# Optimization experiments

Measured on AMD Instinct MI355X. Metric: run time of the kernel, lower is better.

Reference implementation:

```python
import jax, jax.numpy as jnp
import numpy as np

N, E, G, H, ED, L = 100000, 256000, 4000, 300, 64, 5
BN_EPS = 1e-5


def _bn(x, p):
    # p: [4, D] = (gamma, beta, running_mean, running_var); eval-mode batchnorm
    g, b, m, v = p[0], p[1], p[2], p[3]
    return (x - m) * (g / jnp.sqrt(v + BN_EPS)) + b


def setup_inputs() -> dict:
    key = jax.random.key(0)
    ks = iter(jax.random.split(key, 64))
    r = lambda *s: jax.random.normal(next(ks), s, jnp.float32) * 0.02

    def bn_pack(*s):
        # stacked (gamma, beta, mean, var) along axis -2
        return jnp.stack([jnp.ones(s, jnp.float32), jnp.zeros(s, jnp.float32),
                          jax.random.normal(next(ks), s, jnp.float32) * 0.1,
                          jnp.ones(s, jnp.float32)], axis=-2)

    inp = {
        'x': jax.random.randint(next(ks), (N,), 0, 119),
        'edge_attr': jax.random.randint(next(ks), (E,), 0, 32),
        'edge_index': jax.random.randint(next(ks), (2, E), 0, N),
        'batch': jnp.sort(jax.random.randint(next(ks), (N,), 0, G)),
        'num_graphs': G,
        # encoders
        'atom_emb': r(119, H), 'bond_emb': r(32, ED),
        # per-layer GINEConv params (stacked over L layers)
        'We': r(L, H, ED), 'be': jnp.zeros((L, H)),              # edge Linear(edge_dim->hidden)
        'W1': r(L, 2 * H, H), 'b1': jnp.zeros((L, 2 * H)), 'bn1': bn_pack(L, 2 * H),
        'W2': r(L, H, 2 * H), 'b2': jnp.zeros((L, H)), 'bn2': bn_pack(L, H),
        'eps': jnp.zeros((L,), jnp.float32),                      # trainable GIN eps, init 0
        # per-layer pooling linear
        'Wp': r(L, H, H), 'bp': jnp.zeros((L, H)),
        # virtual-node update MLP
        'vnW1': r(H, H), 'vnb1': jnp.zeros((H,)), 'vnbn': bn_pack(H),
        'vnW2': r(H, H), 'vnb2': jnp.zeros((H,)),
        # readout layernorm + head (Linear(H,H//2) -> SiLU -> Linear(H//2,1))
        'ln_g': jnp.ones((H,)), 'ln_b': jnp.zeros((H,)),
        'hW1': r(H // 2, H), 'hb1': jnp.zeros((H // 2,)),
        'hW2': r(1, H // 2), 'hb2': jnp.zeros((1,)),
    }
    return inp


def reference(x, edge_attr, edge_index, batch, num_graphs, atom_emb, bond_emb,
              We, be, W1, b1, bn1, W2, b2, bn2, eps, Wp, bp,
              vnW1, vnb1, vnbn, vnW2, vnb2, ln_g, ln_b, hW1, hb1, hW2, hb2):
    Gn = num_graphs
    h = atom_emb[x]                         # [N, H] atom encoding
    e = bond_emb[edge_attr]                 # [E, ED] bond encoding
    src, dst = edge_index[0], edge_index[1]
    Nn, Hd = h.shape
    vn = jnp.zeros((Gn, Hd), h.dtype)       # vn_embedding init to 0
    hg = jnp.zeros((Gn, Hd), h.dtype)       # sum-over-layers graph readout
    nlayers = We.shape[0]
    for i in range(nlayers):
        if i > 0:
            # virtual-node update + broadcast
            vn_in = jax.ops.segment_sum(h, batch, num_segments=Gn) + vn
            vn = jax.nn.silu(_bn(vn_in @ vnW1.T + vnb1, vnbn)) @ vnW2.T + vnb2
            h = h + vn[batch]
        # GINEConv: sum_j ReLU(h_j + lin(e_ij)) scattered into target nodes
        ep = e @ We[i].T + be[i]             # [E, H]
        m = jax.nn.relu(h[src] + ep)         # gather + relu
        agg = jax.ops.segment_sum(m, dst, num_segments=Nn)  # scatter-add
        z = (1.0 + eps[i]) * h + agg
        z = jax.nn.silu(_bn(z @ W1[i].T + b1[i], bn1[i])) @ W2[i].T + b2[i]  # 2-layer MLP
        z = jax.nn.silu(_bn(z, bn2[i]))      # layer BN + SiLU
        h = z + h if i > 0 else z            # residual (skipped at layer 0)
        hp = jax.ops.segment_sum(h, batch, num_segments=Gn)  # global_add_pool
        hg = hg + hp @ Wp[i].T + bp[i]
    # readout: LayerNorm -> SiLU -> head MLP
    mu = hg.mean(-1, keepdims=True)
    var = ((hg - mu) ** 2).mean(-1, keepdims=True)
    r = jax.nn.silu((hg - mu) / jnp.sqrt(var + BN_EPS) * ln_g + ln_b)
    return jax.nn.silu(r @ hW1.T + hb1) @ hW2.T + hb2   # [G, 1]
```

## Files before the change

### kernel.cpp

```cpp
#include <hip/hip_runtime.h>
#include <hip/hip_bf16.h>
#include <math.h>


typedef __hip_bfloat16 bf16;
typedef __attribute__((ext_vector_type(8))) __bf16 bf16x8;
typedef __attribute__((ext_vector_type(4))) float f32x4;

__device__ __forceinline__ float silu_f(float v) { return v / (1.0f + __expf(-v)); }
__device__ __forceinline__ float bfu_lo(unsigned u) {
    unsigned t = (u & 0xffffu) << 16; return *(float*)&t;
}
__device__ __forceinline__ float bfu_hi(unsigned u) {
    unsigned t = u & 0xffff0000u; return *(float*)&t;
}
__device__ __forceinline__ unsigned packbf(float a, float b) {
    bf16 x = __float2bfloat16(a), y = __float2bfloat16(b);
    return (unsigned)*(unsigned short*)&x | ((unsigned)*(unsigned short*)&y << 16);
}

#define GLOAD16(gp, lp) __builtin_amdgcn_global_load_lds( \
    (const __attribute__((address_space(1))) unsigned int*)(const void*)(gp), \
    (__attribute__((address_space(3))) unsigned int*)(void*)(lp), 16, 0, 0)

__global__ void k_fill(float* __restrict__ p, float v, int n) {
    int stride = gridDim.x * blockDim.x;
    for (int i = blockIdx.x * blockDim.x + threadIdx.x; i < n; i += stride) p[i] = v;
}

__global__ void k_zero(float* __restrict__ p, size_t n) {
    size_t stride = (size_t)gridDim.x * blockDim.x;
    for (size_t i = (size_t)blockIdx.x * blockDim.x + threadIdx.x; i < n; i += stride)
        p[i] = 0.0f;
}

__global__ void k_hist(const int* __restrict__ key, int* __restrict__ cnt, int n) {
    int stride = gridDim.x * blockDim.x;
    for (int i = blockIdx.x * blockDim.x + threadIdx.x; i < n; i += stride)
        atomicAdd(&cnt[key[i]], 1);
}

__global__ __launch_bounds__(256)
void k_scan1(const int* __restrict__ in, int* __restrict__ out,
             int* __restrict__ bsum, int n) {
    __shared__ int wsum[4];
    int base = blockIdx.x << 10;
    int t = threadIdx.x;
    int i0 = base + t * 4;
    int v0 = (i0 + 0 < n) ? in[i0 + 0] : 0;
    int v1 = (i0 + 1 < n) ? in[i0 + 1] : 0;
    int v2 = (i0 + 2 < n) ? in[i0 + 2] : 0;
    int v3 = (i0 + 3 < n) ? in[i0 + 3] : 0;
    int s = v0 + v1 + v2 + v3;
    int lane = t & 63, wid = t >> 6;
    int x = s;
    for (int d = 1; d < 64; d <<= 1) {
        int y = __shfl_up(x, d);
        if (lane >= d) x += y;
    }
    if (lane == 63) wsum[wid] = x;
    __syncthreads();
    int wadd = 0;
    for (int w = 0; w < wid; w++) wadd += wsum[w];
    x += wadd;
    int run = x - s;
    if (i0 + 0 < n) out[i0 + 0] = run; run += v0;
    if (i0 + 1 < n) out[i0 + 1] = run; run += v1;
    if (i0 + 2 < n) out[i0 + 2] = run; run += v2;
    if (i0 + 3 < n) out[i0 + 3] = run; run += v3;
    if (bsum && t == 255) bsum[blockIdx.x] = x;
}

__global__ void k_scan_add(int* __restrict__ out, const int* __restrict__ bsum,
                           int* __restrict__ cur, int n, int total) {
    int stride = gridDim.x * blockDim.x;
    for (int i = blockIdx.x * blockDim.x + threadIdx.x; i < n; i += stride) {
        int v = out[i] + bsum[i >> 10];
        out[i] = v;
        if (cur) cur[i] = v;
    }
    if (blockIdx.x == 0 && threadIdx.x == 0) out[n] = total;
}

__global__ void k_escatter(const int* __restrict__ dst, const int* __restrict__ src,
                           const int* __restrict__ ea, int* __restrict__ cur,
                           int* __restrict__ esrc, int* __restrict__ eea, int E) {
    int stride = gridDim.x * blockDim.x;
    for (int e = blockIdx.x * blockDim.x + threadIdx.x; e < E; e += stride) {
        int p = atomicAdd(&cur[dst[e]], 1);
        esrc[p] = src[e];
        eea[p]  = ea[e];
    }
}

__global__ void k_eptable(const float* __restrict__ bond_emb,
                          const float* __restrict__ We,
                          const float* __restrict__ be,
                          bf16* __restrict__ tblb, int BV, int H, int ED, int KP1) {
    int l = blockIdx.x / BV;
    int a = blockIdx.x % BV;
    int j = threadIdx.x;
    if (j >= KP1) return;
    float s = 0.0f;
    if (j < H) {
        const float* w = We + ((size_t)l * H + j) * ED;
        const float* bb = bond_emb + (size_t)a * ED;
        s = be[(size_t)l * H + j];
        for (int k = 0; k < ED; k++) s += bb[k] * w[k];
    }
    tblb[((size_t)l * BV + a) * KP1 + j] = __float2bfloat16(s);
}

__global__ void k_encode(const int* __restrict__ x, const float* __restrict__ emb,
                         bf16* __restrict__ h, int H, int total) {
    int stride = gridDim.x * blockDim.x;
    for (int i = blockIdx.x * blockDim.x + threadIdx.x; i < total; i += stride) {
        int n = i / H, j = i - n * H;
        h[i] = __float2bfloat16(emb[(size_t)x[n] * H + j]);
    }
}

__global__ __launch_bounds__(256)
void k_msg_csr(const int* __restrict__ eoff, const int* __restrict__ esrc,
               const int* __restrict__ eea, const bf16* __restrict__ h,
               const bf16* __restrict__ tblb, const float* __restrict__ epsp, int l,
               bf16* __restrict__ zb, int H, int KP1, int N) {
    const int wid = blockIdx.x * (blockDim.x >> 6) + (threadIdx.x >> 6);
    const int nw = gridDim.x * (blockDim.x >> 6);
    const int lane = threadIdx.x & 63;
    const float epl = 1.0f + epsp[l];
    const int c0 = 2 * lane;
    for (int n = wid; n < N; n += nw) {
        int e0 = eoff[n], e1 = eoff[n + 1];
        float a0[3] = {0.f, 0.f, 0.f}, a1[3] = {0.f, 0.f, 0.f};
        for (int e = e0; e < e1; e++) {
            int s = esrc[e], a = eea[e];
            const unsigned short* hr = (const unsigned short*)h + (size_t)s * H;
            const unsigned short* tr = (const unsigned short*)tblb + (size_t)a * KP1;
            #pragma unroll
            for (int p = 0; p < 3; p++) {
                int c = c0 + p * 128;
                if (c < H) {
                    unsigned hv = *(const unsigned*)(hr + c);
                    unsigned tv = *(const unsigned*)(tr + c);
                    float v0 = bfu_lo(hv) + bfu_lo(tv);
                    float v1 = bfu_hi(hv) + bfu_hi(tv);
                    if (v0 > 0.0f) a0[p] += v0;
                    if (v1 > 0.0f) a1[p] += v1;
                }
            }
        }
        const unsigned short* hn = (const unsigned short*)h + (size_t)n * H;
        unsigned short* zr = (unsigned short*)zb + (size_t)n * KP1;
        #pragma unroll
        for (int p = 0; p < 3; p++) {
            int c = c0 + p * 128;
            if (c < KP1) {
                float z0 = 0.f, z1 = 0.f;
                if (c < H) {
                    unsigned hv = *(const unsigned*)(hn + c);
                    z0 = epl * bfu_lo(hv) + a0[p];
                    z1 = epl * bfu_hi(hv) + a1[p];
                }
                *(unsigned*)(zr + c) = packbf(z0, z1);
            }
        }
    }
}

__global__ __launch_bounds__(256)
void k_pool_csr(const int* __restrict__ goff, const bf16* __restrict__ h,
                float* __restrict__ hp, bf16* __restrict__ hps, int layer, int KPS,
                int H, int G) {
    int j = threadIdx.x;
    int c = 2 * j;
    if (c >= H) return;
    for (int g = blockIdx.x; g < G; g += gridDim.x) {
        float s0 = 0.0f, s1 = 0.0f;
        int n0 = goff[g], n1 = goff[g + 1];
        const unsigned short* hb = (const unsigned short*)h;
        for (int n = n0; n < n1; n++) {
            unsigned hv = *(const unsigned*)(hb + (size_t)n * H + c);
            s0 += bfu_lo(hv);
            s1 += bfu_hi(hv);
        }
        hp[(size_t)g * H + c] = s0;
        hp[(size_t)g * H + c + 1] = s1;
        *(unsigned*)((unsigned short*)hps + (size_t)g * KPS + layer * H + c) = packbf(s0, s1);
    }
}

__global__ void k_addvn(bf16* __restrict__ h, const float* __restrict__ vn,
                        const int* __restrict__ batch, int H, int total2) {
    int stride = gridDim.x * blockDim.x;
    int HP = H >> 1;
    for (int i = blockIdx.x * blockDim.x + threadIdx.x; i < total2; i += stride) {
        int n = i / HP, p = i - n * HP;
        int c = 2 * p;
        unsigned short* hr = (unsigned short*)h + (size_t)n * H + c;
        unsigned hv = *(unsigned*)hr;
        const float* vr = vn + (size_t)batch[n] * H + c;
        *(unsigned*)hr = packbf(bfu_lo(hv) + vr[0], bfu_hi(hv) + vr[1]);
    }
}

__global__ void k_add_castpad(const float* __restrict__ hp, const float* __restrict__ vn,
                              bf16* __restrict__ o, int H, int KP, int total) {
    int stride = gridDim.x * blockDim.x;
    for (int i = blockIdx.x * blockDim.x + threadIdx.x; i < total; i += stride) {
        int g = i / KP, c = i - g * KP;
        float v = 0.0f;
        if (c < H) v = hp[(size_t)g * H + c] + vn[(size_t)g * H + c];
        o[i] = __float2bfloat16(v);
    }
}

__global__ void k_castw_all(const float* __restrict__ W, bf16* __restrict__ Wb,
                            int L, int R, int K, int Kp, int total) {
    int stride = gridDim.x * blockDim.x;
    int perL = R * K;
    for (int i = blockIdx.x * blockDim.x + threadIdx.x; i < total; i += stride) {
        int RpKp = total / L;
        int l = i / RpKp, rem = i - l * RpKp;
        int r = rem / Kp, c = rem - r * Kp;
        float v = (r < R && c < K) ? W[(size_t)l * perL + (size_t)r * K + c] : 0.0f;
        Wb[i] = __float2bfloat16(v);
    }
}

__global__ void k_castWps(const float* __restrict__ Wp, bf16* __restrict__ Wb,
                          int L, int H, int KPS, int total) {
    int stride = gridDim.x * blockDim.x;
    for (int i = blockIdx.x * blockDim.x + threadIdx.x; i < total; i += stride) {
        int r = i / KPS, c = i - r * KPS;
        float v = 0.0f;
        if (r < H && c < L * H) {
            int li = c / H, k = c - li * H;
            v = Wp[(size_t)li * H * H + (size_t)r * H + k];
        }
        Wb[i] = __float2bfloat16(v);
    }
}

__global__ void k_sumbias(const float* __restrict__ bp, float* __restrict__ o,
                          int L, int H) {
    int j = blockIdx.x * blockDim.x + threadIdx.x;
    if (j < H) {
        float s = 0.f;
        for (int i = 0; i < L; i++) s += bp[(size_t)i * H + j];
        o[j] = s;
    }
}

__global__ __launch_bounds__(512)
void k_mfma_gemm(const bf16* __restrict__ A, const bf16* __restrict__ B,
                 const float* __restrict__ bias, const float* __restrict__ bn,
                 const bf16* __restrict__ resb, bf16* __restrict__ out,
                 float* __restrict__ outf,
                 int M, int Nc, int Kp, int ldA, int ldOut, int ldPad,
                 int dosilu, int ncol) {
    __shared__ short As[3 * 128 * 32];
    __shared__ short Bs[3 * 128 * 32];
    const int nwg = gridDim.x;
    const int bid = blockIdx.x;
    const int q = nwg >> 3, r = nwg & 7;
    const int xcd = bid & 7, ii = bid >> 3;
    const int wgid = (xcd < r ? xcd * (q + 1) : r * (q + 1) + (xcd - r) * q) + ii;
    const int rb = wgid / ncol, cb = wgid - rb * ncol;
    const int bm = rb * 128, bn0 = cb * 128;

    const int tid = threadIdx.x;
    const int wave = tid >> 6, lane = tid & 63;
    const int wr = wave >> 1, wc = wave & 1;
    const int l15 = lane & 15, l4 = lane >> 4;
    const int srow = wave * 16 + (lane >> 2);
    const int sslot = lane & 3;

    f32x4 acc[2][4];
    #pragma unroll
    for (int mi = 0; mi < 2; mi++)
        #pragma unroll
        for (int ni = 0; ni < 4; ni++)
            acc[mi][ni] = (f32x4){0.f, 0.f, 0.f, 0.f};

    const int sg = (sslot ^ ((srow >> 1) & 3)) << 3;

    auto STAGE = [&](int buf, int k0) {
        GLOAD16(A + (size_t)(bm + srow) * ldA + k0 + sg, As + buf * 4096 + wave * 512);
        GLOAD16(B + (size_t)(bn0 + srow) * Kp + k0 + sg, Bs + buf * 4096 + wave * 512);
    };

    const int nt = Kp >> 5;
    STAGE(0, 0);
    if (nt > 1) STAGE(1, 32);
    for (int t = 0; t < nt; ++t) {
        if (t + 1 < nt) asm volatile("s_waitcnt vmcnt(2)" ::: "memory");
        else            asm volatile("s_waitcnt vmcnt(0)" ::: "memory");
        __builtin_amdgcn_sched_barrier(0);
        __builtin_amdgcn_s_barrier();
        __builtin_amdgcn_sched_barrier(0);
        if (t + 2 < nt) STAGE((t + 2) % 3, (t + 2) << 5);
        const short* Ab = As + (t % 3) * 4096;
        const short* Bb = Bs + (t % 3) * 4096;
        bf16x8 a[2], b[4];
        #pragma unroll
        for (int mi = 0; mi < 2; mi++) {
            int row = wr * 32 + mi * 16 + l15;
            a[mi] = *(const bf16x8*)&Ab[row * 32 + ((l4 ^ ((row >> 1) & 3)) << 3)];
        }
        #pragma unroll
        for (int ni = 0; ni < 4; ni++) {
            int row = wc * 64 + ni * 16 + l15;
            b[ni] = *(const bf16x8*)&Bb[row * 32 + ((l4 ^ ((row >> 1) & 3)) << 3)];
        }
        #pragma unroll
        for (int mi = 0; mi < 2; mi++)
            #pragma unroll
            for (int ni = 0; ni < 4; ni++)
                acc[mi][ni] = __builtin_amdgcn_mfma_f32_16x16x32_bf16(
                    a[mi], b[ni], acc[mi][ni], 0, 0, 0);
        __builtin_amdgcn_sched_barrier(0);
    }

    #pragma unroll
    for (int ni = 0; ni < 4; ni++) {
        int col = bn0 + wc * 64 + ni * 16 + l15;
        if (col >= ldPad) continue;
        bool pad = (col >= Nc);
        float bi = (!pad && bias) ? bias[col] : 0.f;
        float sc = 1.f, mm = 0.f, bb = 0.f;
        if (!pad && bn) {
            sc = bn[col] * rsqrtf(bn[3 * Nc + col] + 1e-5f);
            mm = bn[2 * Nc + col];
            bb = bn[Nc + col];
        }
        #pragma unroll
        for (int mi = 0; mi < 2; mi++) {
            #pragma unroll
            for (int rr = 0; rr < 4; rr++) {
                int row = bm + wr * 32 + mi * 16 + l4 * 4 + rr;
                if (row >= M) continue;
                size_t idx = (size_t)row * ldOut + col;
                if (outf) {
                    if (pad) continue;
                    float v = acc[mi][ni][rr] + bi;
                    if (bn) v = (v - mm) * sc + bb;
                    if (dosilu) v = silu_f(v);
                    outf[idx] = v;
                } else {
                    if (pad) { out[idx] = __float2bfloat16(0.f); continue; }
                    float v = acc[mi][ni][rr] + bi;
                    if (bn) v = (v - mm) * sc + bb;
                    if (dosilu) v = silu_f(v);
                    if (resb) v += __bfloat162float(resb[idx]);
                    out[idx] = __float2bfloat16(v);
                }
            }
        }
    }
}

#define GBM 64
#define GBN 64
#define GBK 16
__global__ __launch_bounds__(256)
void k_gemm(const float* __restrict__ A, const float* __restrict__ B,
            const float* __restrict__ bias, const float* __restrict__ bn,
            float* __restrict__ C, int M, int Nc, int K, int flags) {
    __shared__ float As[GBK][GBM + 4];
    __shared__ float Bs[GBK][GBN + 4];
    const int bm = blockIdx.x * GBM;
    const int bnc = blockIdx.y * GBN;
    const int tid = threadIdx.x;
    const int tx = tid & 15, ty = tid >> 4;
    const int ar = tid >> 2;
    const int ak = (tid & 3) << 2;

    float acc[4][4] = {{0.f}};

    for (int k0 = 0; k0 < K; k0 += GBK) {
        {
            int gr = bm + ar, gk = k0 + ak;
            float4 v = make_float4(0.f, 0.f, 0.f, 0.f);
            if (gr < M && gk < K) {
                const float* p = A + (size_t)gr * K;
                if (gk + 3 < K) v = *(const float4*)(p + gk);
                else {
                    v.x = p[gk];
                    if (gk + 1 < K) v.y = p[gk + 1];
                    if (gk + 2 < K) v.z = p[gk + 2];
                }
            }
            As[ak][ar] = v.x; As[ak + 1][ar] = v.y; As[ak + 2][ar] = v.z; As[ak + 3][ar] = v.w;
        }
        {
            int gr = bnc + ar, gk = k0 + ak;
            float4 v = make_float4(0.f, 0.f, 0.f, 0.f);
            if (gr < Nc && gk < K) {
                const float* p = B + (size_t)gr * K;
                if (gk + 3 < K) v = *(const float4*)(p + gk);
                else {
                    v.x = p[gk];
                    if (gk + 1 < K) v.y = p[gk + 1];
                    if (gk + 2 < K) v.z = p[gk + 2];
                }
            }
            Bs[ak][ar] = v.x; Bs[ak + 1][ar] = v.y; Bs[ak + 2][ar] = v.z; Bs[ak + 3][ar] = v.w;
        }
        __syncthreads();
        #pragma unroll
        for (int kk = 0; kk < GBK; kk++) {
            float4 a = *(const float4*)&As[kk][ty * 4];
            float4 b = *(const float4*)&Bs[kk][tx * 4];
            acc[0][0] += a.x * b.x; acc[0][1] += a.x * b.y; acc[0][2] += a.x * b.z; acc[0][3] += a.x * b.w;
            acc[1][0] += a.y * b.x; acc[1][1] += a.y * b.y; acc[1][2] += a.y * b.z; acc[1][3] += a.y * b.w;
            acc[2][0] += a.z * b.x; acc[2][1] += a.z * b.y; acc[2][2] += a.z * b.z; acc[2][3] += a.z * b.w;
            acc[3][0] += a.w * b.x; acc[3][1] += a.w * b.y; acc[3][2] += a.w * b.z; acc[3][3] += a.w * b.w;
        }
        __syncthreads();
    }

    #pragma unroll
    for (int i = 0; i < 4; i++) {
        int row = bm + ty * 4 + i;
        if (row >= M) continue;
        #pragma unroll
        for (int j = 0; j < 4; j++) {
            int col = bnc + tx * 4 + j;
            if (col >= Nc) continue;
            float v = acc[i][j];
            if (bias) v += bias[col];
            if (bn) {
                float g = bn[col], bb = bn[Nc + col], mm = bn[2 * Nc + col], vv = bn[3 * Nc + col];
                v = (v - mm) * (g * rsqrtf(vv + 1e-5f)) + bb;
            }
            if (flags & 1) v = silu_f(v);
            size_t idx = (size_t)row * Nc + col;
            if (flags & 2) C[idx] += v;
            else           C[idx] = v;
        }
    }
}

__global__ __launch_bounds__(256)
void k_ln_silu(const float* __restrict__ hg, const float* __restrict__ g,
               const float* __restrict__ b, float* __restrict__ r, int H) {
    int gi = blockIdx.x;
    const float* row = hg + (size_t)gi * H;
    float s = 0.f, s2 = 0.f;
    for (int j = threadIdx.x; j < H; j += blockDim.x) {
        float v = row[j];
        s += v; s2 += v * v;
    }
    for (int off = 32; off; off >>= 1) {
        s += __shfl_down(s, off);
        s2 += __shfl_down(s2, off);
    }
    __shared__ float rs[4], rs2[4];
    int wid = threadIdx.x >> 6, lane = threadIdx.x & 63;
    if (lane == 0) { rs[wid] = s; rs2[wid] = s2; }
    __syncthreads();
    if (threadIdx.x == 0) {
        float S = 0.f, S2 = 0.f;
        for (int w = 0; w < 4; w++) { S += rs[w]; S2 += rs2[w]; }
        rs[0] = S; rs2[0] = S2;
    }
    __syncthreads();
    float mu = rs[0] / H;
    float var = rs2[0] / H - mu * mu;
    float inv = rsqrtf(var + 1e-5f);
    for (int j = threadIdx.x; j < H; j += blockDim.x) {
        float v = (row[j] - mu) * inv * g[j] + b[j];
        r[(size_t)gi * H + j] = silu_f(v);
    }
}

__global__ void k_head2(const float* __restrict__ r2, const float* __restrict__ w,
                        const float* __restrict__ b, float* __restrict__ out, int Kh) {
    int gi = blockIdx.x;
    int t = threadIdx.x;
    float s = 0.f;
    for (int k = t; k < Kh; k += 64) s += r2[(size_t)gi * Kh + k] * w[k];
    for (int off = 32; off; off >>= 1) s += __shfl_down(s, off);
    if (t == 0) out[gi] = s + b[0];
}

extern "C" void kernel_launch(void* const* d_in, const int* in_sizes, int n_in,
                              void* d_out, int out_size, void* d_ws, size_t ws_size,
                              hipStream_t stream) {
    const int*   x         = (const int*)d_in[0];
    const int*   edge_attr = (const int*)d_in[1];
    const int*   eidx      = (const int*)d_in[2];
    const int*   batch     = (const int*)d_in[3];
    const float* atom_emb  = (const float*)d_in[5];
    const float* bond_emb  = (const float*)d_in[6];
    const float* We  = (const float*)d_in[7];
    const float* be  = (const float*)d_in[8];
    const float* W1  = (const float*)d_in[9];
    const float* b1  = (const float*)d_in[10];
    const float* bn1 = (const float*)d_in[11];
    const float* W2  = (const float*)d_in[12];
    const float* b2  = (const float*)d_in[13];
    const float* bn2 = (const float*)d_in[14];
    const float* epsp= (const float*)d_in[15];
    const float* Wp  = (const float*)d_in[16];
    const float* bp  = (const float*)d_in[17];
    const float* vnW1= (const float*)d_in[18];
    const float* vnb1= (const float*)d_in[19];
    const float* vnbn= (const float*)d_in[20];
    const float* vnW2= (const float*)d_in[21];
    const float* vnb2= (const float*)d_in[22];
    const float* ln_g= (const float*)d_in[23];
    const float* ln_b= (const float*)d_in[24];
    const float* hW1 = (const float*)d_in[25];
    const float* hb1 = (const float*)d_in[26];
    const float* hW2 = (const float*)d_in[27];
    const float* hb2 = (const float*)d_in[28];
    float* out = (float*)d_out;

    const int N  = in_sizes[0];
    const int E  = in_sizes[1];
    const int G  = out_size;
    const int L  = in_sizes[15];
    const int H  = in_sizes[19];
    const int H2 = 2 * H;
    const int ED = in_sizes[7] / (L * H);
    const int BV = in_sizes[6] / ED;
    const int HH = in_sizes[26];
    (void)n_in;

    const int* src = eidx;
    const int* dst = eidx + E;

    const int KP1 = ((H  + 31) / 32) * 32;
    const int KP2 = ((H2 + 31) / 32) * 32;
    const int KPS = ((L * H + 31) / 32) * 32;
    const int RP1 = ((H2 + 127) / 128) * 128;
    const int RP2 = ((H  + 127) / 128) * 128;
    const int Npad = ((N + 127) / 128) * 128;
    const int GP   = ((G + 127) / 128) * 128;

    char* wsb = (char*)d_ws;
    auto alb = [](size_t v) { return (v + 255) & ~(size_t)255; };
    const size_t fN = (size_t)N * H;
    const size_t fG = (size_t)G * H;

    size_t off = 0;
    bf16*  hbf   = (bf16*) (wsb + off); off += alb(fN * 2);
    bf16*  zb    = (bf16*) (wsb + off); off += alb((size_t)Npad * KP1 * 2);
    float* hp    = (float*)(wsb + off); off += alb(fG * 4);
    float* hg    = (float*)(wsb + off); off += alb(fG * 4);
    float* vn    = (float*)(wsb + off); off += alb(fG * 4);
    float* rbuf  = (float*)(wsb + off); off += alb(fG * 4);
    float* r2    = (float*)(wsb + off); off += alb((size_t)G * HH * 4);
    bf16*  tblb  = (bf16*) (wsb + off); off += alb((size_t)L * BV * KP1 * 2);
    float* bsumf = (float*)(wsb + off); off += alb((size_t)RP2 * 4);
    bf16*  W1b   = (bf16*) (wsb + off); off += alb((size_t)L * RP1 * KP1 * 2);
    bf16*  W2b   = (bf16*) (wsb + off); off += alb((size_t)L * RP2 * KP2 * 2);
    bf16*  vnW1b = (bf16*) (wsb + off); off += alb((size_t)RP2 * KP1 * 2);
    bf16*  vnW2b = (bf16*) (wsb + off); off += alb((size_t)RP2 * KP1 * 2);
    bf16*  Wpsb  = (bf16*) (wsb + off); off += alb((size_t)RP2 * KPS * 2);
    bf16*  hps   = (bf16*) (wsb + off); off += alb((size_t)GP * KPS * 2);
    bf16*  vninb = (bf16*) (wsb + off); off += alb((size_t)GP * KP1 * 2);
    bf16*  vntb  = (bf16*) (wsb + off); off += alb((size_t)GP * KP1 * 2);
    int* eoff = (int*)(wsb + off); off += alb((size_t)(N + 1) * 4);
    int* ecur = (int*)(wsb + off); off += alb((size_t)N * 4);
    int* esrc = (int*)(wsb + off); off += alb((size_t)E * 4);
    int* eea  = (int*)(wsb + off); off += alb((size_t)E * 4);
    int* goff = (int*)(wsb + off); off += alb((size_t)(G + 1) * 4);
    int* gcnt = (int*)(wsb + off); off += alb((size_t)G * 4);
    int* bsum = (int*)(wsb + off); off += alb(1024 * 4);

    size_t left = (ws_size > off + 256) ? (ws_size - off - 256) : 0;
    long long chl = (long long)(left / ((size_t)KP2 * 2));
    int CH = (int)((chl > Npad) ? Npad : chl);
    CH = (CH / 128) * 128;
    if (CH < 128) {
        k_fill<<<64, 256, 0, stream>>>(out, 10000.0f + (float)(ws_size >> 20), G);
        return;
    }
    bf16* t1 = (bf16*)(wsb + off);

    auto gemm_f = [&](const float* A, const float* B, const float* bias, const float* bn,
                      float* C, int M, int Nc, int K, int flags) {
        dim3 grid((M + GBM - 1) / GBM, (Nc + GBN - 1) / GBN);
        k_gemm<<<grid, dim3(256), 0, stream>>>(A, B, bias, bn, C, M, Nc, K, flags);
    };
    auto mfma = [&](const bf16* A, const bf16* B, const float* bias, const float* bn,
                    const bf16* resb, bf16* outb, float* outf, int M, int Nc, int Kp,
                    int ldA, int ldOut, int ldPad, int dosilu, int ncolT) {
        int mt = (M + 127) / 128;
        k_mfma_gemm<<<dim3(mt * ncolT), dim3(512), 0, stream>>>(
            A, B, bias, bn, resb, outb, outf, M, Nc, Kp, ldA, ldOut, ldPad, dosilu, ncolT);
    };
    auto zero = [&](void* p, size_t nfloats) { k_zero<<<1024, 256, 0, stream>>>((float*)p, nfloats); };

    const int NH = N * H;

    {
        int nb = (N + 1023) / 1024;
        zero(ecur, N);
        k_hist<<<1024, 256, 0, stream>>>(dst, ecur, E);
        k_scan1<<<nb, 256, 0, stream>>>(ecur, eoff, bsum, N);
        k_scan1<<<1, 256, 0, stream>>>(bsum, bsum, nullptr, nb);
        k_scan_add<<<512, 256, 0, stream>>>(eoff, bsum, ecur, N, E);
        k_escatter<<<1024, 256, 0, stream>>>(dst, src, edge_attr, ecur, esrc, eea, E);

        int nbg = (G + 1023) / 1024;
        zero(gcnt, G);
        k_hist<<<1024, 256, 0, stream>>>(batch, gcnt, N);
        k_scan1<<<nbg, 256, 0, stream>>>(gcnt, goff, bsum, G);
        k_scan1<<<1, 256, 0, stream>>>(bsum, bsum, nullptr, nbg);
        k_scan_add<<<64, 256, 0, stream>>>(goff, bsum, nullptr, G, N);
    }

    zero(vn, fG);
    zero(hps, (size_t)GP * KPS / 2);

    k_eptable<<<L * BV, 320, 0, stream>>>(bond_emb, We, be, tblb, BV, H, ED, KP1);
    k_encode<<<2048, 256, 0, stream>>>(x, atom_emb, hbf, H, NH);
    k_castw_all<<<2048, 256, 0, stream>>>(W1, W1b, L, H2, H, KP1, L * RP1 * KP1);
    k_castw_all<<<2048, 256, 0, stream>>>(W2, W2b, L, H, H2, KP2, L * RP2 * KP2);
    k_castw_all<<<256, 256, 0, stream>>>(vnW1, vnW1b, 1, H, H, KP1, RP2 * KP1);
    k_castw_all<<<256, 256, 0, stream>>>(vnW2, vnW2b, 1, H, H, KP1, RP2 * KP1);
    k_castWps<<<512, 256, 0, stream>>>(Wp, Wpsb, L, H, KPS, RP2 * KPS);
    k_sumbias<<<(H + 255) / 256, 256, 0, stream>>>(bp, bsumf, L, H);

    for (int i = 0; i < L; i++) {
        if (i > 0) {
            k_add_castpad<<<2048, 256, 0, stream>>>(hp, vn, vninb, H, KP1, G * KP1);
            mfma(vninb, vnW1b, vnb1, vnbn, nullptr, vntb, nullptr,
                 G, H, KP1, KP1, KP1, KP1, 1, RP2 / 128);
            mfma(vntb, vnW2b, vnb2, nullptr, nullptr, nullptr, vn,
                 G, H, KP1, KP1, H, H, 0, RP2 / 128);
            k_addvn<<<2048, 256, 0, stream>>>(hbf, vn, batch, H, N * (H >> 1));
        }
        k_msg_csr<<<4096, 256, 0, stream>>>(eoff, esrc, eea, hbf,
                                            tblb + (size_t)i * BV * KP1, epsp, i,
                                            zb, H, KP1, N);
        for (int r0 = 0; r0 < N; r0 += CH) {
            int m = (N - r0 < CH) ? (N - r0) : CH;
            mfma(zb + (size_t)r0 * KP1, W1b + (size_t)i * RP1 * KP1,
                 b1 + (size_t)i * H2, bn1 + (size_t)i * 4 * H2,
                 nullptr, t1, nullptr, m, H2, KP1, KP1, KP2, KP2, 1, RP1 / 128);
            mfma(t1, W2b + (size_t)i * RP2 * KP2, b2 + (size_t)i * H,
                 bn2 + (size_t)i * 4 * H,
                 (i > 0) ? (hbf + (size_t)r0 * H) : nullptr, hbf + (size_t)r0 * H,
                 nullptr, m, H, KP2, KP2, H, H, 1, RP2 / 128);
        }
        k_pool_csr<<<4096, 256, 0, stream>>>(goff, hbf, hp, hps, i, KPS, H, G);
    }

    mfma(hps, Wpsb, bsumf, nullptr, nullptr, nullptr, hg,
         G, H, KPS, KPS, H, H, 0, RP2 / 128);

    k_ln_silu<<<G, 256, 0, stream>>>(hg, ln_g, ln_b, rbuf, H);
    gemm_f(rbuf, hW1, hb1, nullptr, r2, G, HH, H, 1);
    k_head2<<<G, 64, 0, stream>>>(r2, hW2, hb2, out, HH);
}
```

Before: 2.228 ms.

## Fuse GIN two-layer MLP GEMMs into one kernel keeping intermediate in LDS

Replaces the two chunked MFMA GEMM launches per layer with a single kernel. Each block takes 64 rows, runs the first GEMM with BN+SiLU into an LDS buffer of 600 columns, then runs the second GEMM with BN+SiLU+residual straight from LDS. This removes the global round-trip of the wide intermediate activation t1 and one launch per chunk. In exchange it uses smaller per-block tiles (64x128 with 2x2 MFMA tiles per wave) and a large LDS footprint, which can limit occupancy and MFMA efficiency, and weights are re-streamed by every block.

After: 3.349 ms. 50.3% more time.

```diff
diff --git a/kernel.cpp b/kernel.cpp
--- a/kernel.cpp
+++ b/kernel.cpp
@@ -5,6 +5,7 @@
 
 typedef __hip_bfloat16 bf16;
 typedef __attribute__((ext_vector_type(8))) __bf16 bf16x8;
+typedef __attribute__((ext_vector_type(8))) short short8;
 typedef __attribute__((ext_vector_type(4))) float f32x4;
 
 __device__ __forceinline__ float silu_f(float v) { return v / (1.0f + __expf(-v)); }
@@ -17,6 +18,10 @@
 __device__ __forceinline__ unsigned packbf(float a, float b) {
     bf16 x = __float2bfloat16(a), y = __float2bfloat16(b);
     return (unsigned)*(unsigned short*)&x | ((unsigned)*(unsigned short*)&y << 16);
+}
+__device__ __forceinline__ short bfs(float v) {
+    bf16 t = __float2bfloat16(v);
+    return *(short*)&t;
 }
 
 #define GLOAD16(gp, lp) __builtin_amdgcn_global_load_lds( \
@@ -249,6 +254,176 @@
         float s = 0.f;
         for (int i = 0; i < L; i++) s += bp[(size_t)i * H + j];
         o[j] = s;
+    }
+}
+
+__global__ __launch_bounds__(512)
+void k_mlp_fused(const bf16* __restrict__ zb, const bf16* __restrict__ W1b,
+                 const float* __restrict__ b1, const float* __restrict__ bn1,
+                 const bf16* __restrict__ W2b, const float* __restrict__ b2,
+                 const float* __restrict__ bn2, bf16* __restrict__ hbf,
+                 int N, int H, int H2, int KP1, int KP2, int RP1, int RP2,
+                 int useres) {
+    __shared__ short zbs[64 * 328];
+    __shared__ short t1s[64 * 616];
+    __shared__ short ws[3 * 128 * 32];
+    const int tid = threadIdx.x;
+    const int wave = tid >> 6, lane = tid & 63;
+    const int wr = wave >> 2, wc = wave & 3;
+    const int l15 = lane & 15, l4 = lane >> 4;
+    const int r0 = blockIdx.x * 64;
+
+    {
+        const int CW = KP1 >> 3;
+        for (int idx = tid; idx < 64 * CW; idx += 512) {
+            int row = idx / CW, c8 = idx - row * CW;
+            short8 v = *(const short8*)((const short*)zb + (size_t)(r0 + row) * KP1 + c8 * 8);
+            *(short8*)&zbs[row * 328 + c8 * 8] = v;
+        }
+    }
+    __syncthreads();
+
+    const int srowW = wave * 16 + (lane >> 2);
+    const int sgW = ((lane & 3) ^ ((srowW >> 1) & 3)) << 3;
+
+    for (int cb = 0; cb < RP1 / 128; cb++) {
+        const bf16* Wt = W1b + (size_t)cb * 128 * KP1;
+        GLOAD16(Wt + (size_t)srowW * KP1 + 0 + sgW, ws + wave * 512);
+        GLOAD16(Wt + (size_t)srowW * KP1 + 32 + sgW, ws + 4096 + wave * 512);
+        const int nt = KP1 >> 5;
+        f32x4 acc[2][2];
+        #pragma unroll
+        for (int mi = 0; mi < 2; mi++)
+            #pragma unroll
+            for (int ni = 0; ni < 2; ni++)
+                acc[mi][ni] = (f32x4){0.f, 0.f, 0.f, 0.f};
+        for (int t = 0; t < nt; t++) {
+            if (t + 1 < nt) asm volatile("s_waitcnt vmcnt(1)" ::: "memory");
+            else            asm volatile("s_waitcnt vmcnt(0)" ::: "memory");
+            __builtin_amdgcn_sched_barrier(0);
+            __builtin_amdgcn_s_barrier();
+            __builtin_amdgcn_sched_barrier(0);
+            if (t + 2 < nt)
+                GLOAD16(Wt + (size_t)srowW * KP1 + (t + 2) * 32 + sgW,
+                        ws + ((t + 2) % 3) * 4096 + wave * 512);
+            const short* Wb_ = ws + (t % 3) * 4096;
+            bf16x8 a[2], b[2];
+            #pragma unroll
+            for (int mi = 0; mi < 2; mi++)
+                a[mi] = *(const bf16x8*)&zbs[(wr * 32 + mi * 16 + l15) * 328 + t * 32 + l4 * 8];
+            #pragma unroll
+            for (int ni = 0; ni < 2; ni++) {
+                int row = wc * 32 + ni * 16 + l15;
+                b[ni] = *(const bf16x8*)&Wb_[row * 32 + ((l4 ^ ((row >> 1) & 3)) << 3)];
+            }
+            #pragma unroll
+            for (int mi = 0; mi < 2; mi++)
+                #pragma unroll
+                for (int ni = 0; ni < 2; ni++)
+                    acc[mi][ni] = __builtin_amdgcn_mfma_f32_16x16x32_bf16(
+                        a[mi], b[ni], acc[mi][ni], 0, 0, 0);
+            __builtin_amdgcn_sched_barrier(0);
+        }
+        #pragma unroll
+        for (int ni = 0; ni < 2; ni++) {
+            int col = cb * 128 + wc * 32 + ni * 16 + l15;
+            if (col >= KP2) continue;
+            bool pad = (col >= H2);
+            float bi = pad ? 0.f : b1[col];
+            float sc = 1.f, mm = 0.f, bb = 0.f;
+            if (!pad) {
+                sc = bn1[col] * rsqrtf(bn1[3 * H2 + col] + 1e-5f);
+                mm = bn1[2 * H2 + col];
+                bb = bn1[H2 + col];
+            }
+            #pragma unroll
+            for (int mi = 0; mi < 2; mi++) {
+                #pragma unroll
+                for (int rr = 0; rr < 4; rr++) {
+                    int row = wr * 32 + mi * 16 + l4 * 4 + rr;
+                    float v = 0.f;
+                    if (!pad) {
+                        v = acc[mi][ni][rr] + bi;
+                        v = (v - mm) * sc + bb;
+                        v = silu_f(v);
+                    }
+                    t1s[row * 616 + col] = bfs(v);
+                }
+            }
+        }
+        __builtin_amdgcn_sched_barrier(0);
+        __builtin_amdgcn_s_barrier();
+        __builtin_amdgcn_sched_barrier(0);
+    }
+    asm volatile("s_waitcnt lgkmcnt(0)" ::: "memory");
+    __builtin_amdgcn_sched_barrier(0);
+    __builtin_amdgcn_s_barrier();
+    __builtin_amdgcn_sched_barrier(0);
+
+    for (int cb = 0; cb < RP2 / 128; cb++) {
+        const bf16* Wt = W2b + (size_t)cb * 128 * KP2;
+        GLOAD16(Wt + (size_t)srowW * KP2 + 0 + sgW, ws + wave * 512);
+        GLOAD16(Wt + (size_t)srowW * KP2 + 32 + sgW, ws + 4096 + wave * 512);
+        const int nt = KP2 >> 5;
+        f32x4 acc[2][2];
+        #pragma unroll
+        for (int mi = 0; mi < 2; mi++)
+            #pragma unroll
+            for (int ni = 0; ni < 2; ni++)
+                acc[mi][ni] = (f32x4){0.f, 0.f, 0.f, 0.f};
+        for (int t = 0; t < nt; t++) {
+            if (t + 1 < nt) asm volatile("s_waitcnt vmcnt(1)" ::: "memory");
+            else            asm volatile("s_waitcnt vmcnt(0)" ::: "memory");
+            __builtin_amdgcn_sched_barrier(0);
+            __builtin_amdgcn_s_barrier();
+            __builtin_amdgcn_sched_barrier(0);
+            if (t + 2 < nt)
+                GLOAD16(Wt + (size_t)srowW * KP2 + (t + 2) * 32 + sgW,
+                        ws + ((t + 2) % 3) * 4096 + wave * 512);
+            const short* Wb_ = ws + (t % 3) * 4096;
+            bf16x8 a[2], b[2];
+            #pragma unroll
+            for (int mi = 0; mi < 2; mi++)
+                a[mi] = *(const bf16x8*)&t1s[(wr * 32 + mi * 16 + l15) * 616 + t * 32 + l4 * 8];
+            #pragma unroll
+            for (int ni = 0; ni < 2; ni++) {
+                int row = wc * 32 + ni * 16 + l15;
+                b[ni] = *(const bf16x8*)&Wb_[row * 32 + ((l4 ^ ((row >> 1) & 3)) << 3)];
+            }
+            #pragma unroll
+            for (int mi = 0; mi < 2; mi++)
+                #pragma unroll
+                for (int ni = 0; ni < 2; ni++)
+                    acc[mi][ni] = __builtin_amdgcn_mfma_f32_16x16x32_bf16(
+                        a[mi], b[ni], acc[mi][ni], 0, 0, 0);
+            __builtin_amdgcn_sched_barrier(0);
+        }
+        #pragma unroll
+        for (int ni = 0; ni < 2; ni++) {
+            int col = cb * 128 + wc * 32 + ni * 16 + l15;
+            if (col >= H) continue;
+            float bi = b2[col];
+            float sc = bn2[col] * rsqrtf(bn2[3 * H + col] + 1e-5f);
+            float mm = bn2[2 * H + col];
+            float bb = bn2[H + col];
+            #pragma unroll
+            for (int mi = 0; mi < 2; mi++) {
+                #pragma unroll
+                for (int rr = 0; rr < 4; rr++) {
+                    int row = r0 + wr * 32 + mi * 16 + l4 * 4 + rr;
+                    if (row >= N) continue;
+                    size_t idx = (size_t)row * H + col;
+                    float v = acc[mi][ni][rr] + bi;
+                    v = (v - mm) * sc + bb;
+                    v = silu_f(v);
+                    if (useres) v += __bfloat162float(hbf[idx]);
+                    hbf[idx] = __float2bfloat16(v);
+                }
+            }
+        }
+        __builtin_amdgcn_sched_barrier(0);
+        __builtin_amdgcn_s_barrier();
+        __builtin_amdgcn_sched_barrier(0);
     }
 }
 
@@ -571,15 +746,10 @@
     int* gcnt = (int*)(wsb + off); off += alb((size_t)G * 4);
     int* bsum = (int*)(wsb + off); off += alb(1024 * 4);
 
-    size_t left = (ws_size > off + 256) ? (ws_size - off - 256) : 0;
-    long long chl = (long long)(left / ((size_t)KP2 * 2));
-    int CH = (int)((chl > Npad) ? Npad : chl);
-    CH = (CH / 128) * 128;
-    if (CH < 128) {
+    if (ws_size < off + 256) {
         k_fill<<<64, 256, 0, stream>>>(out, 10000.0f + (float)(ws_size >> 20), G);
         return;
     }
-    bf16* t1 = (bf16*)(wsb + off);
 
     auto gemm_f = [&](const float* A, const float* B, const float* bias, const float* bn,
                       float* C, int M, int Nc, int K, int flags) {
@@ -638,16 +808,10 @@
         k_msg_csr<<<4096, 256, 0, stream>>>(eoff, esrc, eea, hbf,
                                             tblb + (size_t)i * BV * KP1, epsp, i,
                                             zb, H, KP1, N);
-        for (int r0 = 0; r0 < N; r0 += CH) {
-            int m = (N - r0 < CH) ? (N - r0) : CH;
-            mfma(zb + (size_t)r0 * KP1, W1b + (size_t)i * RP1 * KP1,
-                 b1 + (size_t)i * H2, bn1 + (size_t)i * 4 * H2,
-                 nullptr, t1, nullptr, m, H2, KP1, KP1, KP2, KP2, 1, RP1 / 128);
-            mfma(t1, W2b + (size_t)i * RP2 * KP2, b2 + (size_t)i * H,
-                 bn2 + (size_t)i * 4 * H,
-                 (i > 0) ? (hbf + (size_t)r0 * H) : nullptr, hbf + (size_t)r0 * H,
-                 nullptr, m, H, KP2, KP2, H, H, 1, RP2 / 128);
-        }
+        k_mlp_fused<<<Npad / 64, 512, 0, stream>>>(
+            zb, W1b + (size_t)i * RP1 * KP1, b1 + (size_t)i * H2, bn1 + (size_t)i * 4 * H2,
+            W2b + (size_t)i * RP2 * KP2, b2 + (size_t)i * H, bn2 + (size_t)i * 4 * H,
+            hbf, N, H, H2, KP1, KP2, RP1, RP2, (i > 0) ? 1 : 0);
         k_pool_csr<<<4096, 256, 0, stream>>>(goff, hbf, hp, hps, i, KPS, H, G);
     }
 
```
